# Optimization experiments

Hardware: AMD Instinct MI355X
Metric: run time of the kernel (lower is better)

The kernel has to match this reference:

```python
import jax, jax.numpy as jnp
import numpy as np

N = 2048        # nodes
IN_DIM = 128    # input feature dim
K = 8           # channels
D = 32          # per-channel dim (C_dim)
ITERS = 4       # routing iterations
BETA = 1.0      # attention temperature
EPS = 1e-12     # F.normalize eps


def l2norm(x):
    # F.normalize(x, dim=-1): x / max(||x||_2, eps)
    n = jnp.linalg.norm(x, axis=-1, keepdims=True)
    return x / jnp.maximum(n, EPS)


def setup_inputs() -> dict:
    key = jax.random.key(0)
    k1, k2, k3, k4 = jax.random.split(key, 4)
    adj = jax.random.randint(k1, (N, N), 0, 2, dtype=jnp.int32)
    features = jax.random.normal(k2, (N, IN_DIM), dtype=jnp.float32)
    # parameters initialized ~ N(0,1) as in init_parameters
    W = jax.random.normal(k3, (K, IN_DIM, D), dtype=jnp.float32)
    b = jax.random.normal(k4, (K, D), dtype=jnp.float32)
    return {"adj": adj, "features": features, "W": W, "b": b}


def reference(adj, features, W, b):
    mask = (adj > 0)[None, :, :]                         # [1, N, N]
    # per-channel projection + row L2 normalize -> Z: [K, N, D]
    Z = l2norm(jnp.einsum('nd,kdc->knc', features, W) + b[:, None, :])
    for _ in range(ITERS):
        # per-channel masked attention scores [K, N, N]
        att = jnp.einsum('knc,kmc->knm', Z, Z)
        att = jnp.where(mask, att, 0.0) / BETA
        # softmax across channels (dim=2 in torch after cat == K axis here)
        att = jax.nn.softmax(att, axis=0)
        att = jnp.where(mask, att, 0.0)
        # weighted aggregate + residual + L2 normalize
        Z = l2norm(Z + jnp.einsum('knm,kmc->knc', att, Z))
    # concat channels along feature dim -> [N, K*D]
    return jnp.transpose(Z, (1, 0, 2)).reshape(N, K * D)
```

## Files before the change

### kernel.cpp

```cpp
#include <hip/hip_runtime.h>
#include <hip/hip_bf16.h>
#include <hip/hip_fp16.h>

#define NN 2048
#define KK 8
#define DD 32
#define ZSZ (KK * NN * DD)
#define ZS2 (KK * NN * 16)
#define PSTR 20
#define NCH 16

typedef __attribute__((ext_vector_type(8))) short short8;
typedef __attribute__((ext_vector_type(4))) float f32x4;
typedef __attribute__((ext_vector_type(4))) unsigned int u32x4;

union UU { u32x4 q; short8 v; unsigned int u[4]; };

#define SELHI 0x07060302u
#define SELLO 0x05040100u

__device__ __forceinline__ unsigned int prm(unsigned int a, unsigned int b, unsigned int sel) {
  return __builtin_amdgcn_perm(a, b, sel);
}
__device__ __forceinline__ unsigned int bfr(float x) {
  unsigned int u = __float_as_uint(x);
  return (u + 0x7fffu + ((u >> 16) & 1u)) >> 16;
}
__device__ __forceinline__ unsigned int packp(float a, float b) {
  union { __hip_bfloat162 h; unsigned int u; } cv;
  cv.h = __float22bfloat162_rn(make_float2(a, b));
  return cv.u;
}
__device__ __forceinline__ unsigned int packh(float a, float b) {
  union { __half2 h; unsigned int u; } cv;
  cv.h = __float22half2_rn(make_float2(a, b));
  return cv.u;
}
__device__ __forceinline__ float2 unpackh(unsigned int u) {
  union { unsigned int u; __half2 h; } cv;
  cv.u = u;
  return __half22float2(cv.h);
}
__device__ __forceinline__ f32x4 MF(short8 a, short8 b, f32x4 c) {
  return __builtin_amdgcn_mfma_f32_16x16x32_bf16(a, b, c, 0, 0, 0);
}
__device__ __forceinline__ short8 as_s8(u32x4 x) { UU u; u.q = x; return u.v; }

__global__ __launch_bounds__(256) void pm_kernel(const float* __restrict__ feat,
                                                 const float* __restrict__ W,
                                                 const float* __restrict__ bias,
                                                 float* __restrict__ Z,
                                                 unsigned short* __restrict__ Zghi,
                                                 unsigned short* __restrict__ Zthi,
                                                 const int* __restrict__ adj,
                                                 unsigned int* __restrict__ mbits) {
  const int t = threadIdx.x;
  if (blockIdx.x < 256) {
    const int nb = blockIdx.x * 8;
    const int k = t >> 5, c = t & 31;
    float s[8];
#pragma unroll
    for (int j = 0; j < 8; ++j) s[j] = bias[k * DD + c];
    const float* w = W + (k * 128) * DD + c;
    const float* fp = feat + nb * 128;
#pragma unroll 4
    for (int d = 0; d < 128; ++d) {
      float wv = w[d * DD];
#pragma unroll
      for (int j = 0; j < 8; ++j) s[j] = fmaf(fp[j * 128 + d], wv, s[j]);
    }
    unsigned int hi[8];
#pragma unroll
    for (int j = 0; j < 8; ++j) {
      float sq = s[j] * s[j];
#pragma unroll
      for (int off = 16; off > 0; off >>= 1) sq += __shfl_xor(sq, off, 32);
      float z = s[j] / fmaxf(sqrtf(sq), 1e-12f);
      Z[(k * NN + nb + j) * DD + c] = z;
      hi[j] = bfr(z);
      Zghi[(k * NN + nb + j) * DD + c] = (unsigned short)hi[j];
    }
    uint4 tp = make_uint4(hi[0] | (hi[1] << 16), hi[2] | (hi[3] << 16),
                          hi[4] | (hi[5] << 16), hi[6] | (hi[7] << 16));
    *(uint4*)&Zthi[(size_t)k * DD * NN + (size_t)c * NN + nb] = tp;
  } else {
    const int base = (blockIdx.x - 256) * 1024 + t;
    const int lane = t & 63;
    int v[4];
#pragma unroll
    for (int rr = 0; rr < 4; ++rr) v[rr] = adj[base + 256 * rr];
#pragma unroll
    for (int rr = 0; rr < 4; ++rr) {
      int idx = base + 256 * rr;
      unsigned long long b = __ballot(v[rr] > 0);
      if (lane == 0) mbits[idx >> 5] = (unsigned int)b;
      if (lane == 32) mbits[idx >> 5] = (unsigned int)(b >> 32);
    }
  }
}

template <int NCt>
__global__ __launch_bounds__(256) void rp_kernel(const float* __restrict__ Zin,
                                                 const unsigned int* __restrict__ partU,
                                                 float* __restrict__ Zout,
                                                 unsigned short* __restrict__ Zghi,
                                                 unsigned short* __restrict__ Zthi) {
  __shared__ unsigned short T[DD][33];
  const int t = threadIdx.x;
  const int k = blockIdx.x >> 6, mt = blockIdx.x & 63;
  const int m0 = mt * 32;
  const int mloc = t >> 3, c4 = t & 7;
  const size_t idx = (size_t)(k * NN + m0 + mloc) * DD + 4 * c4;
  float4 v = *(const float4*)&Zin[idx];
#pragma unroll
  for (int j = 0; j < NCt; ++j) {
    uint2 pp = *(const uint2*)&partU[(size_t)j * ZS2 + (size_t)(k * NN + m0 + mloc) * 16 + 2 * c4];
    float2 f0 = unpackh(pp.x), f1 = unpackh(pp.y);
    v.x += f0.x; v.y += f0.y; v.z += f1.x; v.w += f1.y;
  }
  float sq = v.x * v.x + v.y * v.y + v.z * v.z + v.w * v.w;
  sq += __shfl_xor(sq, 1, 8);
  sq += __shfl_xor(sq, 2, 8);
  sq += __shfl_xor(sq, 4, 8);
  const float sc = 1.0f / fmaxf(sqrtf(sq), 1e-12f);
  float z[4] = {v.x * sc, v.y * sc, v.z * sc, v.w * sc};
  *(float4*)&Zout[idx] = make_float4(z[0], z[1], z[2], z[3]);
  unsigned int hi[4];
#pragma unroll
  for (int e = 0; e < 4; ++e) {
    hi[e] = bfr(z[e]);
    T[4 * c4 + e][mloc] = (unsigned short)hi[e];
  }
  *(uint2*)&Zghi[idx] = make_uint2(hi[0] | (hi[1] << 16), hi[2] | (hi[3] << 16));
  __syncthreads();
  const int cloc = t >> 3, m4 = t & 7;
  unsigned int o0 = (unsigned int)T[cloc][4 * m4 + 0] | ((unsigned int)T[cloc][4 * m4 + 1] << 16);
  unsigned int o1 = (unsigned int)T[cloc][4 * m4 + 2] | ((unsigned int)T[cloc][4 * m4 + 3] << 16);
  *(uint2*)&Zthi[(size_t)k * DD * NN + (size_t)cloc * NN + m0 + 4 * m4] = make_uint2(o0, o1);
}

template <int NS>
__global__ __launch_bounds__(256, 2) void iter_kernel(const unsigned short* __restrict__ Zghi,
                                                      const unsigned short* __restrict__ Zthi,
                                                      const unsigned int* __restrict__ mbits,
                                                      unsigned int* __restrict__ partU) {
  __shared__ __align__(16) unsigned int lds[2 * 8192 + 4 * 16 * PSTR];
  const int t = threadIdx.x;
  const int w = t >> 6;
  const int lane = t & 63;
  const int l15 = lane & 15;
  const int g = lane >> 4;
  const int nw = blockIdx.x * 64 + w * 16;
  const int mchunk = blockIdx.y * (NS * 32);

  const unsigned int* Zg = (const unsigned int*)Zghi;
  const unsigned int* Zt = (const unsigned int*)Zthi;

  const int srow = lane >> 2;
  const int sq4 = (lane & 3) * 4;
  auto issue_loads = [&](int b, int mb) {
#pragma unroll
    for (int j = 0; j < 4; ++j) {
      int chunk = 4 * w + j;
      int row = chunk * 16 + srow;
      int k = row >> 5, rm = row & 31;
      __builtin_amdgcn_global_load_lds(
          (const unsigned int*)&Zg[(size_t)k * (NN * 16) + (size_t)(mb + rm) * 16 + sq4],
          &lds[b * 8192 + chunk * 256], 16, 0, 0);
      __builtin_amdgcn_global_load_lds(
          (const unsigned int*)&Zt[(size_t)k * (NN * 16) + (size_t)rm * (NN / 2) + (mb >> 1) + sq4],
          &lds[b * 8192 + 4096 + chunk * 256], 16, 0, 0);
    }
  };

  short8 A[KK];
#pragma unroll
  for (int k = 0; k < KK; ++k)
    A[k] = as_s8(*(const u32x4*)&Zg[(size_t)(k * NN + nw + l15) * 16 + 4 * g]);

  unsigned int mwa[4][NS];
#pragma unroll
  for (int r = 0; r < 4; ++r) {
    uint4 m4 = *(const uint4*)&mbits[(size_t)(nw + 4 * g + r) * 64 + (mchunk >> 5)];
    mwa[r][0] = m4.x; mwa[r][1] = m4.y; mwa[r][2] = m4.z; mwa[r][3] = m4.w;
  }

  f32x4 O[KK][2];
#pragma unroll
  for (int k = 0; k < KK; ++k)
#pragma unroll
    for (int ch = 0; ch < 2; ++ch) O[k][ch] = {0.0f, 0.0f, 0.0f, 0.0f};

  issue_loads(0, mchunk);

  unsigned int* Pw = &lds[16384 + w * (16 * PSTR)];

#pragma unroll
  for (int st = 0; st < NS; ++st) {
    __syncthreads();
    if (st + 1 < NS) issue_loads((st + 1) & 1, mchunk + (st + 1) * 32);
    const unsigned int* buf = &lds[(st & 1) * 8192];

    unsigned int pp[4][2][4];
#pragma unroll
    for (int sub = 0; sub < 2; ++sub) {
      f32x4 S[KK];
#pragma unroll
      for (int k = 0; k < KK; ++k) {
        int m = 16 * sub + l15;
        u32x4 bh = *(const u32x4*)&buf[(k * 32 + m) * 16 + 4 * g];
        f32x4 z = {0.0f, 0.0f, 0.0f, 0.0f};
        S[k] = MF(A[k], as_s8(bh), z);
      }
#pragma unroll
      for (int r = 0; r < 4; ++r) {
        float e[KK];
        float sum = 0.0f;
#pragma unroll
        for (int k = 0; k < KK; ++k) { e[k] = __expf(S[k][r]); sum += e[k]; }
        int ml = 16 * sub + l15;
        float f = ((mwa[r][st] >> ml) & 1u) ? __builtin_amdgcn_rcpf(sum) : 0.0f;
#pragma unroll
        for (int k = 0; k < KK; ++k) S[k][r] = e[k] * f;
#pragma unroll
        for (int kp = 0; kp < 4; ++kp)
          pp[kp][sub][r] = packp(S[2 * kp][r], S[2 * kp + 1][r]);
      }
    }

#pragma unroll
    for (int kp = 0; kp < 4; ++kp) {
#pragma unroll
      for (int sub = 0; sub < 2; ++sub)
#pragma unroll
        for (int r = 0; r < 4; ++r)
          Pw[(4 * g + r) * PSTR + 16 * sub + l15] = pp[kp][sub][r];

      const unsigned int* Pr = &Pw[l15 * PSTR + 8 * g];
      u32x4 a0 = *(const u32x4*)Pr;
      u32x4 a1 = *(const u32x4*)(Pr + 4);
      UU pk0, pk1;
      pk0.u[0] = prm(a0.y, a0.x, SELLO); pk0.u[1] = prm(a0.w, a0.z, SELLO);
      pk0.u[2] = prm(a1.y, a1.x, SELLO); pk0.u[3] = prm(a1.w, a1.z, SELLO);
      pk1.u[0] = prm(a0.y, a0.x, SELHI); pk1.u[1] = prm(a0.w, a0.z, SELHI);
      pk1.u[2] = prm(a1.y, a1.x, SELHI); pk1.u[3] = prm(a1.w, a1.z, SELHI);
#pragma unroll
      for (int kk = 0; kk < 2; ++kk) {
        int k = 2 * kp + kk;
#pragma unroll
        for (int ch = 0; ch < 2; ++ch) {
          int c = 16 * ch + l15;
          u32x4 b = *(const u32x4*)&buf[4096 + (k * 32 + c) * 16 + 4 * g];
          O[k][ch] = MF(kk ? pk1.v : pk0.v, as_s8(b), O[k][ch]);
        }
      }
    }
  }

  unsigned int* dst = partU + (size_t)blockIdx.y * ZS2;
  const int even = ((l15 & 1) == 0);
#pragma unroll
  for (int k = 0; k < KK; ++k)
#pragma unroll
    for (int ch = 0; ch < 2; ++ch) {
      f32x4 o = O[k][ch];
#pragma unroll
      for (int r = 0; r < 4; ++r) {
        float partner = __shfl_xor(o[r], 1);
        if (even) {
          dst[(size_t)(k * NN + nw + 4 * g + r) * 16 + ((16 * ch + l15) >> 1)] =
              packh(o[r], partner);
        }
      }
    }
}

template <int NCt>
__global__ __launch_bounds__(256) void ro_kernel(const float* __restrict__ Zin,
                                                 const unsigned int* __restrict__ partU,
                                                 float* __restrict__ out) {
  const int n = blockIdx.x, t = threadIdx.x;
  const int k = t >> 5, c = t & 31;
  float v = Zin[(size_t)(k * NN + n) * DD + c];
#pragma unroll
  for (int j = 0; j < NCt; ++j) {
    unsigned int pu = partU[(size_t)j * ZS2 + (size_t)(k * NN + n) * 16 + (c >> 1)];
    float2 f = unpackh(pu);
    v += (c & 1) ? f.y : f.x;
  }
  float sq = v * v;
#pragma unroll
  for (int off = 16; off > 0; off >>= 1) sq += __shfl_xor(sq, off, 32);
  out[n * (KK * DD) + t] = v / fmaxf(sqrtf(sq), 1e-12f);
}

extern "C" void kernel_launch(void* const* d_in, const int* in_sizes, int n_in,
                              void* d_out, int out_size, void* d_ws, size_t ws_size,
                              hipStream_t stream) {
  const int* adj = (const int*)d_in[0];
  const float* feat = (const float*)d_in[1];
  const float* W = (const float*)d_in[2];
  const float* b = (const float*)d_in[3];
  float* out = (float*)d_out;

  float* Z0 = (float*)d_ws;
  float* Z1 = Z0 + ZSZ;
  unsigned short* Zghi = (unsigned short*)(Z1 + ZSZ);
  unsigned short* Zthi = Zghi + ZSZ;
  unsigned int* mbits = (unsigned int*)(Zthi + ZSZ);
  unsigned int* partU = mbits + NN * 64;

  pm_kernel<<<256 + 4096, 256, 0, stream>>>(feat, W, b, Z0, Zghi, Zthi, adj, mbits);

  float* zi = Z0;
  float* zo = Z1;
  for (int it = 0; it < 4; ++it) {
    iter_kernel<4><<<dim3(32, NCH), 256, 0, stream>>>(Zghi, Zthi, mbits, partU);
    if (it < 3) {
      rp_kernel<NCH><<<512, 256, 0, stream>>>(zi, partU, zo, Zghi, Zthi);
      float* tmp = zi; zi = zo; zo = tmp;
    } else {
      ro_kernel<NCH><<<NN, 256, 0, stream>>>(zi, partU, out);
    }
  }
}
```

Measured before the change: 201.0 us.

## Replace block-shared async LDS double buffer with per-wave synchronous 16-column staging

New measurement: 291.6 us. +45.1%, slower.

```diff
diff --git a/kernel.cpp b/kernel.cpp
--- a/kernel.cpp
+++ b/kernel.cpp
@@ -139,49 +139,35 @@
   *(uint2*)&Zthi[(size_t)k * DD * NN + (size_t)cloc * NN + m0 + 4 * m4] = make_uint2(o0, o1);
 }
 
-template <int NS>
 __global__ __launch_bounds__(256, 2) void iter_kernel(const unsigned short* __restrict__ Zghi,
                                                       const unsigned short* __restrict__ Zthi,
                                                       const unsigned int* __restrict__ mbits,
                                                       unsigned int* __restrict__ partU) {
-  __shared__ __align__(16) unsigned int lds[2 * 8192 + 4 * 16 * PSTR];
+  __shared__ __align__(16) unsigned int lds[16384 + 4 * 16 * PSTR];
   const int t = threadIdx.x;
   const int w = t >> 6;
   const int lane = t & 63;
   const int l15 = lane & 15;
   const int g = lane >> 4;
   const int nw = blockIdx.x * 64 + w * 16;
-  const int mchunk = blockIdx.y * (NS * 32);
+  const int chunk = blockIdx.y * 128;
 
   const unsigned int* Zg = (const unsigned int*)Zghi;
   const unsigned int* Zt = (const unsigned int*)Zthi;
 
-  const int srow = lane >> 2;
-  const int sq4 = (lane & 3) * 4;
-  auto issue_loads = [&](int b, int mb) {
-#pragma unroll
-    for (int j = 0; j < 4; ++j) {
-      int chunk = 4 * w + j;
-      int row = chunk * 16 + srow;
-      int k = row >> 5, rm = row & 31;
-      __builtin_amdgcn_global_load_lds(
-          (const unsigned int*)&Zg[(size_t)k * (NN * 16) + (size_t)(mb + rm) * 16 + sq4],
-          &lds[b * 8192 + chunk * 256], 16, 0, 0);
-      __builtin_amdgcn_global_load_lds(
-          (const unsigned int*)&Zt[(size_t)k * (NN * 16) + (size_t)rm * (NN / 2) + (mb >> 1) + sq4],
-          &lds[b * 8192 + 4096 + chunk * 256], 16, 0, 0);
-    }
-  };
+  unsigned int* bufG = &lds[w * 2048];
+  unsigned int* bufT = &lds[8192 + w * 2048];
+  unsigned int* Pw = &lds[16384 + w * (16 * PSTR)];
 
   short8 A[KK];
 #pragma unroll
   for (int k = 0; k < KK; ++k)
     A[k] = as_s8(*(const u32x4*)&Zg[(size_t)(k * NN + nw + l15) * 16 + 4 * g]);
 
-  unsigned int mwa[4][NS];
+  unsigned int mwa[4][4];
 #pragma unroll
   for (int r = 0; r < 4; ++r) {
-    uint4 m4 = *(const uint4*)&mbits[(size_t)(nw + 4 * g + r) * 64 + (mchunk >> 5)];
+    uint4 m4 = *(const uint4*)&mbits[(size_t)(nw + 4 * g + r) * 64 + (chunk >> 5)];
     mwa[r][0] = m4.x; mwa[r][1] = m4.y; mwa[r][2] = m4.z; mwa[r][3] = m4.w;
   }
 
@@ -191,54 +177,60 @@
 #pragma unroll
     for (int ch = 0; ch < 2; ++ch) O[k][ch] = {0.0f, 0.0f, 0.0f, 0.0f};
 
-  issue_loads(0, mchunk);
-
-  unsigned int* Pw = &lds[16384 + w * (16 * PSTR)];
-
-#pragma unroll
-  for (int st = 0; st < NS; ++st) {
-    __syncthreads();
-    if (st + 1 < NS) issue_loads((st + 1) & 1, mchunk + (st + 1) * 32);
-    const unsigned int* buf = &lds[(st & 1) * 8192];
-
-    unsigned int pp[4][2][4];
-#pragma unroll
-    for (int sub = 0; sub < 2; ++sub) {
-      f32x4 S[KK];
-#pragma unroll
-      for (int k = 0; k < KK; ++k) {
-        int m = 16 * sub + l15;
-        u32x4 bh = *(const u32x4*)&buf[(k * 32 + m) * 16 + 4 * g];
-        f32x4 z = {0.0f, 0.0f, 0.0f, 0.0f};
-        S[k] = MF(A[k], as_s8(bh), z);
+  const int tc = lane >> 1, tp_ = lane & 1;
+
+#pragma unroll
+  for (int st = 0; st < 8; ++st) {
+    const int mb = chunk + st * 16;
+
+#pragma unroll
+    for (int j = 0; j < 8; ++j) {
+      u32x4 vg = *(const u32x4*)&Zg[(size_t)(j * NN + mb) * 16 + 4 * lane];
+      *(u32x4*)&bufG[j * 256 + 4 * lane] = vg;
+      u32x4 vt = *(const u32x4*)&Zt[(size_t)j * (DD * NN / 2) + (size_t)tc * (NN / 2) +
+                                    (mb >> 1) + 4 * tp_];
+      *(u32x4*)&bufT[j * 256 + tc * 8 + 4 * tp_] = vt;
+    }
+
+    f32x4 S[KK];
+#pragma unroll
+    for (int k = 0; k < KK; ++k) {
+      u32x4 bh = *(const u32x4*)&bufG[(k * 16 + l15) * 16 + 4 * g];
+      f32x4 z = {0.0f, 0.0f, 0.0f, 0.0f};
+      S[k] = MF(A[k], as_s8(bh), z);
+    }
+
+    const int sh = ((mb & 31)) + l15;
+#pragma unroll
+    for (int r = 0; r < 4; ++r) {
+      float e[KK];
+      float sum = 0.0f;
+#pragma unroll
+      for (int k = 0; k < KK; ++k) { e[k] = __expf(S[k][r]); sum += e[k]; }
+      float f = ((mwa[r][st >> 1] >> sh) & 1u) ? __builtin_amdgcn_rcpf(sum) : 0.0f;
+#pragma unroll
+      for (int k = 0; k < KK; ++k) S[k][r] = e[k] * f;
+    }
+    unsigned int pp[4][4];
+#pragma unroll
+    for (int r = 0; r < 4; ++r)
+#pragma unroll
+      for (int kp = 0; kp < 4; ++kp)
+        pp[kp][r] = packp(S[2 * kp][r], S[2 * kp + 1][r]);
+
+#pragma unroll
+    for (int kp = 0; kp < 4; ++kp) {
+#pragma unroll
+      for (int r = 0; r < 4; ++r)
+        Pw[(4 * g + r) * PSTR + l15] = pp[kp][r];
+
+      const int gr = g & 1;
+      u32x4 a0 = *(const u32x4*)&Pw[l15 * PSTR + 8 * gr];
+      u32x4 a1 = *(const u32x4*)&Pw[l15 * PSTR + 8 * gr + 4];
+      if (g >= 2) {
+        a0 = {0u, 0u, 0u, 0u};
+        a1 = {0u, 0u, 0u, 0u};
       }
-#pragma unroll
-      for (int r = 0; r < 4; ++r) {
-        float e[KK];
-        float sum = 0.0f;
-#pragma unroll
-        for (int k = 0; k < KK; ++k) { e[k] = __expf(S[k][r]); sum += e[k]; }
-        int ml = 16 * sub + l15;
-        float f = ((mwa[r][st] >> ml) & 1u) ? __builtin_amdgcn_rcpf(sum) : 0.0f;
-#pragma unroll
-        for (int k = 0; k < KK; ++k) S[k][r] = e[k] * f;
-#pragma unroll
-        for (int kp = 0; kp < 4; ++kp)
-          pp[kp][sub][r] = packp(S[2 * kp][r], S[2 * kp + 1][r]);
-      }
-    }
-
-#pragma unroll
-    for (int kp = 0; kp < 4; ++kp) {
-#pragma unroll
-      for (int sub = 0; sub < 2; ++sub)
-#pragma unroll
-        for (int r = 0; r < 4; ++r)
-          Pw[(4 * g + r) * PSTR + 16 * sub + l15] = pp[kp][sub][r];
-
-      const unsigned int* Pr = &Pw[l15 * PSTR + 8 * g];
-      u32x4 a0 = *(const u32x4*)Pr;
-      u32x4 a1 = *(const u32x4*)(Pr + 4);
       UU pk0, pk1;
       pk0.u[0] = prm(a0.y, a0.x, SELLO); pk0.u[1] = prm(a0.w, a0.z, SELLO);
       pk0.u[2] = prm(a1.y, a1.x, SELLO); pk0.u[3] = prm(a1.w, a1.z, SELLO);
@@ -250,7 +242,7 @@
 #pragma unroll
         for (int ch = 0; ch < 2; ++ch) {
           int c = 16 * ch + l15;
-          u32x4 b = *(const u32x4*)&buf[4096 + (k * 32 + c) * 16 + 4 * g];
+          u32x4 b = *(const u32x4*)&bufT[(k * 32 + c) * 8 + 4 * gr];
           O[k][ch] = MF(kk ? pk1.v : pk0.v, as_s8(b), O[k][ch]);
         }
       }
@@ -315,7 +307,7 @@
   float* zi = Z0;
   float* zo = Z1;
   for (int it = 0; it < 4; ++it) {
-    iter_kernel<4><<<dim3(32, NCH), 256, 0, stream>>>(Zghi, Zthi, mbits, partU);
+    iter_kernel<<<dim3(32, NCH), 256, 0, stream>>>(Zghi, Zthi, mbits, partU);
     if (it < 3) {
       rp_kernel<NCH><<<512, 256, 0, stream>>>(zi, partU, zo, Zghi, Zthi);
       float* tmp = zi; zi = zo; zo = tmp;
```
